# Kernel tuning notes

Measured on AMD Instinct MI355X. Metric: run time of the kernel, lower is better.

The kernel has to match this reference:

```python
import jax, jax.numpy as jnp
import numpy as np

# dims: N sentences, L tokens each, M=2 memory slots/sentence, D hidden, H heads
N, L, M, D, H, FF, V, P, LAYERS = 4, 256, 2, 768, 12, 3072, 32000, 1024, 4
DH = D // H


def setup_inputs() -> dict:
    key = jax.random.key(0)
    ks = jax.random.split(key, 20)
    s = 0.02
    inp = {
        'input_ids': jax.random.randint(ks[0], (N, L), 0, V),
        'memory': jax.random.normal(ks[1], (N, M, D), jnp.float32),
        'emb_table': jax.random.normal(ks[2], (V, D), jnp.float32) * s,
        'pos_table': jax.random.normal(ks[3], (P + 2, D), jnp.float32) * s,
        'Wq': jax.random.normal(ks[4], (LAYERS, D, D), jnp.float32) * s,
        'bq': jnp.zeros((LAYERS, D), jnp.float32),
        'Wk': jax.random.normal(ks[5], (LAYERS, D, D), jnp.float32) * s,
        'bk': jnp.zeros((LAYERS, D), jnp.float32),
        'Wv': jax.random.normal(ks[6], (LAYERS, D, D), jnp.float32) * s,
        'bv': jnp.zeros((LAYERS, D), jnp.float32),
        'W1': jax.random.normal(ks[7], (LAYERS, D, FF), jnp.float32) * s,
        'b1': jnp.zeros((LAYERS, FF), jnp.float32),
        'W2': jax.random.normal(ks[8], (LAYERS, FF, D), jnp.float32) * s,
        'b2': jnp.zeros((LAYERS, D), jnp.float32),
        'g1': jnp.ones((LAYERS, D), jnp.float32),
        'be1': jnp.zeros((LAYERS, D), jnp.float32),
        'g2': jnp.ones((LAYERS, D), jnp.float32),
        'be2': jnp.zeros((LAYERS, D), jnp.float32),
    }
    return inp


def _layer_norm(x, g, b):
    mu = jnp.mean(x, axis=-1, keepdims=True)
    var = jnp.mean((x - mu) ** 2, axis=-1, keepdims=True)
    return (x - mu) / jnp.sqrt(var + 1e-5) * g + b


def _encoder(input_ids, memory, emb_table, pos_table, Wq, bq, Wk, bk, Wv, bv,
             W1, b1, W2, b2, g1, be1, g2, be2):
    base = N * M            # token rows start here in the packed input
    T = base + N * L        # total rows (memory rows + token rows)
    Kk = M + L              # keys per query (own memory + own tokens)

    # position embeddings: memory rows get pos (p % M); tokens get id_pos + M
    mem_pos = jnp.tile(jnp.arange(M), N)                    # (N*M,)
    mem = memory.reshape(N * M, D) + pos_table[mem_pos]
    fwd_pos = jnp.tile(jnp.arange(L) + M, N)                # (N*L,)
    tok = emb_table[input_ids.reshape(-1)] + pos_table[fwd_pos]
    x = jnp.concatenate([mem, tok], axis=0)                 # (T, D)

    # per-sentence key set: its M memory rows then its L token rows
    key_pos = jnp.concatenate([
        jnp.arange(N)[:, None] * M + jnp.arange(M)[None, :],
        base + jnp.arange(N)[:, None] * L + jnp.arange(L)[None, :],
    ], axis=1)                                              # (N, Kk)
    sent = jnp.concatenate([jnp.repeat(jnp.arange(N), M),
                            jnp.repeat(jnp.arange(N), L)])  # (T,)
    gidx = key_pos[sent]                                    # (T, Kk)
    # equal-length sentences => the additive mask built by the torch code is
    # all zeros (key_len == max_key_len for every row), so it is omitted.

    scale = 1.0 / np.sqrt(DH)
    for i in range(LAYERS):
        # K/V are linear row-wise, so project once on all rows then gather
        # (identical math to projecting the gathered tgt, without T-fold GEMM)
        q = (x @ Wq[i] + bq[i]).reshape(T, H, DH)
        kf = (x @ Wk[i] + bk[i]).reshape(T, H, DH)
        vf = (x @ Wv[i] + bv[i]).reshape(T, H, DH)
        kg = kf[gidx]                                       # (T, Kk, H, DH)
        vg = vf[gidx]
        scores = jnp.einsum('thd,tkhd->thk', q, kg) * scale
        probs = jax.nn.softmax(scores, axis=-1)
        ctx = jnp.einsum('thk,tkhd->thd', probs, vg).reshape(T, D)
        x = _layer_norm(x + ctx, g1[i], be1[i])
        h = jax.nn.gelu(x @ W1[i] + b1[i], approximate=False)
        x = _layer_norm(x + h @ W2[i] + b2[i], g2[i], be2[i])

    ret = key_pos[:, M:]                                    # (N, L) token rows
    return x[ret]                                           # (N, L, D)


def reference(input_ids, memory, emb_table, pos_table, Wq, bq, Wk, bk, Wv, bv,
              W1, b1, W2, b2, g1, be1, g2, be2):
    return _encoder(input_ids, memory, emb_table, pos_table, Wq, bq, Wk, bk,
                    Wv, bv, W1, b1, W2, b2, g1, be1, g2, be2)
```

## Files before the change

### kernel.cpp

```cpp
#include <hip/hip_runtime.h>
#include <hip/hip_bf16.h>
#include <math.h>

#define N_      4
#define L_      256
#define M_      2
#define D_      768
#define H_      12
#define FF_     3072
#define DH_     64
#define LAYERS_ 4
#define BASE_   8
#define T_      1032
#define TP_     1088
#define KK_     258
#define QS_     2304
#define PS_     264

typedef __bf16 bf16x8 __attribute__((ext_vector_type(8)));
typedef float  f32x4  __attribute__((ext_vector_type(4)));

__device__ __forceinline__ void async_load16(const __hip_bfloat16* g, __hip_bfloat16* l) {
  __builtin_amdgcn_global_load_lds(
      (const __attribute__((address_space(1))) unsigned int*)g,
      (__attribute__((address_space(3))) unsigned int*)l, 16, 0, 0);
}

#define PP_QKV_END_ 6912
#define PP_W1_END_  16128
#define PP_W2_END_  25344
#define PP_B_END_   25380
#define PP_TOTAL_   26412

__global__ __launch_bounds__(256) void preprocess_kernel(
    const float* __restrict__ Wq, const float* __restrict__ Wk,
    const float* __restrict__ Wv, const float* __restrict__ W1,
    const float* __restrict__ W2,
    const float* __restrict__ bq, const float* __restrict__ bk,
    const float* __restrict__ bv,
    const int* __restrict__ ids, const float* __restrict__ memory,
    const float* __restrict__ emb, const float* __restrict__ pos,
    __hip_bfloat16* __restrict__ Wqkvt, __hip_bfloat16* __restrict__ W1t,
    __hip_bfloat16* __restrict__ W2t, float* __restrict__ bqkv,
    float* __restrict__ x, __hip_bfloat16* __restrict__ xb) {
  __shared__ float tile[32][33];
  const int bid = blockIdx.x;
  const int tid = threadIdx.x;

  const float* src;
  __hip_bfloat16* dst;
  int K, N, bx, by;

  if (bid < PP_QKV_END_) {
    int l = bid / 1728, r = bid - l * 1728;
    int which = r / 576; r -= which * 576;
    by = r / 24; bx = r - by * 24;
    src = (which == 0 ? Wq : which == 1 ? Wk : Wv) + (size_t)l * D_ * D_;
    dst = Wqkvt + (size_t)l * QS_ * D_ + (size_t)which * D_ * D_;
    K = D_; N = D_;
  } else if (bid < PP_W1_END_) {
    int r0 = bid - PP_QKV_END_;
    int l = r0 / 2304, r = r0 - l * 2304;
    by = r / 96; bx = r - by * 96;
    src = W1 + (size_t)l * D_ * FF_;
    dst = W1t + (size_t)l * FF_ * D_;
    K = D_; N = FF_;
  } else if (bid < PP_W2_END_) {
    int r0 = bid - PP_W1_END_;
    int l = r0 / 2304, r = r0 - l * 2304;
    by = r / 24; bx = r - by * 24;
    src = W2 + (size_t)l * FF_ * D_;
    dst = W2t + (size_t)l * D_ * FF_;
    K = FF_; N = D_;
  } else if (bid < PP_B_END_) {
    int i = (bid - PP_W2_END_) * 256 + tid;
    int l = i / QS_, j = i - l * QS_;
    float v;
    if (j < D_)            v = bq[l * D_ + j];
    else if (j < 2 * D_)   v = bk[l * D_ + (j - D_)];
    else                   v = bv[l * D_ + (j - 2 * D_)];
    bqkv[i] = v;
    return;
  } else {
    int row = bid - PP_B_END_;
    const float *s2, *p;
    if (row < BASE_) {
      s2 = memory + (long long)row * D_;
      p  = pos + (row & 1) * D_;
    } else {
      int i = row - BASE_;
      int tok = ids[i];
      s2 = emb + (long long)tok * D_;
      p  = pos + (M_ + (i & (L_ - 1))) * D_;
    }
    for (int d = tid; d < D_; d += 256) {
      float v = s2[d] + p[d];
      x[(long long)row * D_ + d]  = v;
      xb[(long long)row * D_ + d] = __float2bfloat16(v);
    }
    return;
  }

  const int k0 = by * 32, n0 = bx * 32;
  const int r = tid >> 5, c = tid & 31;
  #pragma unroll
  for (int i = 0; i < 4; ++i)
    tile[r + i * 8][c] = src[(size_t)(k0 + r + i * 8) * N + n0 + c];
  __syncthreads();
  #pragma unroll
  for (int i = 0; i < 4; ++i)
    dst[(size_t)(n0 + r + i * 8) * K + k0 + c] = __float2bfloat16(tile[c][r + i * 8]);
}

template <int ACT, int WF32, int WBF16, int WVT>
__global__ __launch_bounds__(256) void gemm_mfma(
    const __hip_bfloat16* __restrict__ A,
    const __hip_bfloat16* __restrict__ Bt,
    const float* __restrict__ bias,
    float* __restrict__ C,
    __hip_bfloat16* __restrict__ Cb,
    __hip_bfloat16* __restrict__ vt,
    int N, int K) {
  __shared__ __align__(16) __hip_bfloat16 As[4][64][32];
  __shared__ __align__(16) __hip_bfloat16 Bs[4][64][32];
  const int tid  = threadIdx.x;
  const int lane = tid & 63, wid = tid >> 6;
  const int ln   = lane & 15, qd = lane >> 4;
  const int wm   = wid >> 1, wn = wid & 1;

  const size_t arow = (size_t)(blockIdx.y * 64 + wid * 16 + (lane >> 2)) * K + (lane & 3) * 8;
  const size_t brow = (size_t)(blockIdx.x * 64 + wid * 16 + (lane >> 2)) * K + (lane & 3) * 8;

  f32x4 acc[2][2] = {};
  for (int k0 = 0; k0 < K; k0 += 128) {
    #pragma unroll
    for (int s = 0; s < 4; ++s) {
      async_load16(A  + arow + k0 + s * 32, &As[s][wid * 16][0]);
      async_load16(Bt + brow + k0 + s * 32, &Bs[s][wid * 16][0]);
    }
    __syncthreads();
    #pragma unroll
    for (int s = 0; s < 4; ++s) {
      bf16x8 a0 = *(const bf16x8*)&As[s][wm * 32 + ln][qd * 8];
      bf16x8 a1 = *(const bf16x8*)&As[s][wm * 32 + 16 + ln][qd * 8];
      bf16x8 b0 = *(const bf16x8*)&Bs[s][wn * 32 + ln][qd * 8];
      bf16x8 b1 = *(const bf16x8*)&Bs[s][wn * 32 + 16 + ln][qd * 8];
      acc[0][0] = __builtin_amdgcn_mfma_f32_16x16x32_bf16(a0, b0, acc[0][0], 0, 0, 0);
      acc[0][1] = __builtin_amdgcn_mfma_f32_16x16x32_bf16(a0, b1, acc[0][1], 0, 0, 0);
      acc[1][0] = __builtin_amdgcn_mfma_f32_16x16x32_bf16(a1, b0, acc[1][0], 0, 0, 0);
      acc[1][1] = __builtin_amdgcn_mfma_f32_16x16x32_bf16(a1, b1, acc[1][1], 0, 0, 0);
    }
    __syncthreads();
  }
  #pragma unroll
  for (int mt = 0; mt < 2; ++mt) {
    #pragma unroll
    for (int nt = 0; nt < 2; ++nt) {
      const int col = blockIdx.x * 64 + wn * 32 + nt * 16 + ln;
      const float bv = bias[col];
      #pragma unroll
      for (int i = 0; i < 4; ++i) {
        const int row = blockIdx.y * 64 + wm * 32 + mt * 16 + qd * 4 + i;
        float v = acc[mt][nt][i] + bv;
        if (ACT) v = 0.5f * v * (1.f + erff(v * 0.70710678118654752f));
        if (WF32)  C[(size_t)row * N + col]  = v;
        if (WVT) {
          if (col < 2 * D_) Cb[(size_t)row * N + col] = __float2bfloat16(v);
          else              vt[(size_t)(col - 2 * D_) * TP_ + row] = __float2bfloat16(v);
        } else if (WBF16) {
          Cb[(size_t)row * N + col] = __float2bfloat16(v);
        }
      }
    }
  }
}

__global__ __launch_bounds__(256) void attn_mfma(
    const __hip_bfloat16* __restrict__ qkv,
    const __hip_bfloat16* __restrict__ vtb,
    float* __restrict__ ctx) {
  __shared__ __align__(16) __hip_bfloat16 Ps[64][PS_];
  const int qt = blockIdx.x, h = blockIdx.y, b = blockIdx.z;
  const int tid = threadIdx.x;
  const int w = tid >> 6, lane = tid & 63, ln = lane & 15, qd = lane >> 4;

  bf16x8 aq0, aq1;
  {
    int j = qt * 64 + w * 16 + ln;
    int tok = (j < 256) ? (BASE_ + b * L_ + j)
            : ((j < KK_) ? (b * M_ + (j - 256)) : (b * M_));
    const __hip_bfloat16* qp = qkv + (size_t)tok * QS_ + h * DH_ + qd * 8;
    aq0 = *(const bf16x8*)qp;
    aq1 = *(const bf16x8*)(qp + 32);
  }

  f32x4 sa[17];
  #pragma unroll
  for (int nt = 0; nt < 17; ++nt) sa[nt] = (f32x4){0.f, 0.f, 0.f, 0.f};
  #pragma unroll
  for (int nt = 0; nt < 17; ++nt) {
    int key = nt * 16 + ln;
    int ktok = (key < 256) ? (BASE_ + b * L_ + key)
             : ((key < KK_) ? (b * M_ + (key - 256)) : (b * M_));
    const __hip_bfloat16* kp = qkv + (size_t)ktok * QS_ + D_ + h * DH_ + qd * 8;
    bf16x8 b0 = *(const bf16x8*)kp;
    bf16x8 b1 = *(const bf16x8*)(kp + 32);
    sa[nt] = __builtin_amdgcn_mfma_f32_16x16x32_bf16(aq0, b0, sa[nt], 0, 0, 0);
    sa[nt] = __builtin_amdgcn_mfma_f32_16x16x32_bf16(aq1, b1, sa[nt], 0, 0, 0);
  }

  #pragma unroll
  for (int i = 0; i < 4; ++i) {
    float v[17];
    #pragma unroll
    for (int nt = 0; nt < 17; ++nt) v[nt] = sa[nt][i] * 0.125f;
    float mx = -1e30f;
    #pragma unroll
    for (int nt = 0; nt < 16; ++nt) mx = fmaxf(mx, v[nt]);
    if (ln < 2) mx = fmaxf(mx, v[16]);
    #pragma unroll
    for (int m = 1; m < 16; m <<= 1) mx = fmaxf(mx, __shfl_xor(mx, m));
    float sum = 0.f;
    #pragma unroll
    for (int nt = 0; nt < 17; ++nt) {
      float e = (nt == 16 && ln >= 2) ? 0.f : __expf(v[nt] - mx);
      v[nt] = e;
      sum += e;
    }
    #pragma unroll
    for (int m = 1; m < 16; m <<= 1) sum += __shfl_xor(sum, m);
    float is = 1.f / sum;
    const int row = w * 16 + qd * 4 + i;
    #pragma unroll
    for (int nt = 0; nt < 17; ++nt)
      if (nt < 16 || ln < 2)
        Ps[row][nt * 16 + ln] = __float2bfloat16(v[nt] * is);
  }

  f32x4 oa[4] = {};
  #pragma unroll
  for (int k0 = 0; k0 < 8; ++k0) {
    bf16x8 ap = *(const bf16x8*)&Ps[w * 16 + ln][k0 * 32 + qd * 8];
    #pragma unroll
    for (int nt = 0; nt < 4; ++nt) {
      const __hip_bfloat16* vp = vtb + (size_t)(h * DH_ + nt * 16 + ln) * TP_
                               + BASE_ + b * L_ + k0 * 32 + qd * 8;
      bf16x8 bv = *(const bf16x8*)vp;
      oa[nt] = __builtin_amdgcn_mfma_f32_16x16x32_bf16(ap, bv, oa[nt], 0, 0, 0);
    }
  }
  {
    float p0[4], p1[4];
    #pragma unroll
    for (int i = 0; i < 4; ++i) {
      p0[i] = __bfloat162float(Ps[w * 16 + qd * 4 + i][256]);
      p1[i] = __bfloat162float(Ps[w * 16 + qd * 4 + i][257]);
    }
    #pragma unroll
    for (int nt = 0; nt < 4; ++nt) {
      const __hip_bfloat16* vp = vtb + (size_t)(h * DH_ + nt * 16 + ln) * TP_ + b * M_;
      float v0 = __bfloat162float(vp[0]);
      float v1 = __bfloat162float(vp[1]);
      #pragma unroll
      for (int i = 0; i < 4; ++i) oa[nt][i] += p0[i] * v0 + p1[i] * v1;
    }
  }

  #pragma unroll
  for (int i = 0; i < 4; ++i) {
    int j = qt * 64 + w * 16 + qd * 4 + i;
    if (j < KK_) {
      int tok = (j < 256) ? (BASE_ + b * L_ + j) : (b * M_ + (j - 256));
      #pragma unroll
      for (int nt = 0; nt < 4; ++nt)
        ctx[(size_t)tok * D_ + h * DH_ + nt * 16 + ln] = oa[nt][i];
    }
  }
}

__global__ __launch_bounds__(256) void add_ln_kernel(
    float* __restrict__ x, const float* __restrict__ delta,
    const float* __restrict__ g, const float* __restrict__ b,
    __hip_bfloat16* __restrict__ xb, float* __restrict__ out) {
  __shared__ float sred[4];
  __shared__ float sbc;
  const int t = blockIdx.x, tid = threadIdx.x;
  float y[3];
  float s = 0.f;
  #pragma unroll
  for (int i = 0; i < 3; ++i) {
    int d = tid + i * 256;
    y[i] = x[(long long)t * D_ + d] + delta[(long long)t * D_ + d];
    s += y[i];
  }
  #pragma unroll
  for (int o = 32; o > 0; o >>= 1) s += __shfl_down(s, o);
  if ((tid & 63) == 0) sred[tid >> 6] = s;
  __syncthreads();
  if (tid == 0) sbc = (sred[0] + sred[1] + sred[2] + sred[3]) * (1.f / D_);
  __syncthreads();
  const float mu = sbc;
  __syncthreads();
  float vs = 0.f;
  #pragma unroll
  for (int i = 0; i < 3; ++i) { float d = y[i] - mu; vs += d * d; }
  #pragma unroll
  for (int o = 32; o > 0; o >>= 1) vs += __shfl_down(vs, o);
  if ((tid & 63) == 0) sred[tid >> 6] = vs;
  __syncthreads();
  if (tid == 0) sbc = (sred[0] + sred[1] + sred[2] + sred[3]) * (1.f / D_);
  __syncthreads();
  const float inv = rsqrtf(sbc + 1e-5f);
  #pragma unroll
  for (int i = 0; i < 3; ++i) {
    int d = tid + i * 256;
    float v = (y[i] - mu) * inv * g[d] + b[d];
    x[(long long)t * D_ + d]  = v;
    xb[(long long)t * D_ + d] = __float2bfloat16(v);
    if (out != nullptr && t >= BASE_)
      out[(size_t)(t - BASE_) * D_ + d] = v;
  }
}

extern "C" void kernel_launch(void* const* d_in, const int* in_sizes, int n_in,
                              void* d_out, int out_size, void* d_ws, size_t ws_size,
                              hipStream_t stream) {
  const int*   ids    = (const int*)  d_in[0];
  const float* memory = (const float*)d_in[1];
  const float* emb    = (const float*)d_in[2];
  const float* pos    = (const float*)d_in[3];
  const float* Wq     = (const float*)d_in[4];
  const float* bq     = (const float*)d_in[5];
  const float* Wk     = (const float*)d_in[6];
  const float* bk     = (const float*)d_in[7];
  const float* Wv     = (const float*)d_in[8];
  const float* bv     = (const float*)d_in[9];
  const float* W1     = (const float*)d_in[10];
  const float* b1     = (const float*)d_in[11];
  const float* W2     = (const float*)d_in[12];
  const float* b2     = (const float*)d_in[13];
  const float* g1     = (const float*)d_in[14];
  const float* be1    = (const float*)d_in[15];
  const float* g2     = (const float*)d_in[16];
  const float* be2    = (const float*)d_in[17];

  char* w = (char*)d_ws;
  float* x    = (float*)w;                      w += (size_t)TP_ * D_ * 4;
  float* cb   = (float*)w;                      w += (size_t)TP_ * D_ * 4;
  float* bqkv = (float*)w;                      w += (size_t)LAYERS_ * QS_ * 4;
  __hip_bfloat16* xb    = (__hip_bfloat16*)w;   w += (size_t)TP_ * D_ * 2;
  __hip_bfloat16* qkvb  = (__hip_bfloat16*)w;   w += (size_t)TP_ * QS_ * 2;
  __hip_bfloat16* vtb   = (__hip_bfloat16*)w;   w += (size_t)D_ * TP_ * 2;
  __hip_bfloat16* hbb   = (__hip_bfloat16*)w;   w += (size_t)TP_ * FF_ * 2;
  __hip_bfloat16* Wqkvt = (__hip_bfloat16*)w;   w += (size_t)LAYERS_ * QS_ * D_ * 2;
  __hip_bfloat16* W1t   = (__hip_bfloat16*)w;   w += (size_t)LAYERS_ * FF_ * D_ * 2;
  __hip_bfloat16* W2t   = (__hip_bfloat16*)w;   w += (size_t)LAYERS_ * D_ * FF_ * 2;

  preprocess_kernel<<<PP_TOTAL_, 256, 0, stream>>>(
      Wq, Wk, Wv, W1, W2, bq, bk, bv, ids, memory, emb, pos,
      Wqkvt, W1t, W2t, bqkv, x, xb);

  for (int i = 0; i < LAYERS_; ++i) {
    gemm_mfma<0, 0, 1, 1><<<dim3(QS_ / 64, TP_ / 64), 256, 0, stream>>>(
        xb, Wqkvt + (size_t)i * QS_ * D_, bqkv + i * QS_, nullptr, qkvb, vtb, QS_, D_);
    attn_mfma<<<dim3(5, H_, N_), 256, 0, stream>>>(qkvb, vtb, cb);
    add_ln_kernel<<<T_, 256, 0, stream>>>(x, cb, g1 + i * D_, be1 + i * D_, xb, nullptr);
    gemm_mfma<1, 0, 1, 0><<<dim3(FF_ / 64, TP_ / 64), 256, 0, stream>>>(
        xb, W1t + (size_t)i * FF_ * D_, b1 + i * FF_, nullptr, hbb, nullptr, FF_, D_);
    gemm_mfma<0, 1, 0, 0><<<dim3(D_ / 64, TP_ / 64), 256, 0, stream>>>(
        hbb, W2t + (size_t)i * D_ * FF_, b2 + i * D_, cb, nullptr, nullptr, D_, FF_);
    add_ln_kernel<<<T_, 256, 0, stream>>>(
        x, cb, g2 + i * D_, be2 + i * D_, xb,
        (i == LAYERS_ - 1) ? (float*)d_out : nullptr);
  }
}
```

Measured before the change: 562.5 us.

## Double-buffer GEMM LDS staging and split-K the W2 projection

Adds a second LDS buffer so the next 128-wide K tile is loaded asynchronously while MFMAs consume the current one. The W2 GEMM is additionally split into two K halves across blockIdx.z, writing separate fp32 partials. The following add+layernorm kernel sums them, which raises block count for the small-N GEMM. This costs doubled LDS per block, an extra partial buffer, and extra memory traffic in the layernorm.

```diff
diff --git a/kernel.cpp b/kernel.cpp
--- a/kernel.cpp
+++ b/kernel.cpp
@@ -112,7 +112,7 @@
     dst[(size_t)(n0 + r + i * 8) * K + k0 + c] = __float2bfloat16(tile[c][r + i * 8]);
 }
 
-template <int ACT, int WF32, int WBF16, int WVT>
+template <int ACT, int WF32, int WBF16, int WVT, int NSPLIT>
 __global__ __launch_bounds__(256) void gemm_mfma(
     const __hip_bfloat16* __restrict__ A,
     const __hip_bfloat16* __restrict__ Bt,
@@ -120,50 +120,64 @@
     float* __restrict__ C,
     __hip_bfloat16* __restrict__ Cb,
     __hip_bfloat16* __restrict__ vt,
-    int N, int K) {
-  __shared__ __align__(16) __hip_bfloat16 As[4][64][32];
-  __shared__ __align__(16) __hip_bfloat16 Bs[4][64][32];
+    int N, int Ktot) {
+  __shared__ __align__(16) __hip_bfloat16 As[2][4][64][32];
+  __shared__ __align__(16) __hip_bfloat16 Bs[2][4][64][32];
   const int tid  = threadIdx.x;
   const int lane = tid & 63, wid = tid >> 6;
   const int ln   = lane & 15, qd = lane >> 4;
   const int wm   = wid >> 1, wn = wid & 1;
 
-  const size_t arow = (size_t)(blockIdx.y * 64 + wid * 16 + (lane >> 2)) * K + (lane & 3) * 8;
-  const size_t brow = (size_t)(blockIdx.x * 64 + wid * 16 + (lane >> 2)) * K + (lane & 3) * 8;
+  const int K = Ktot / NSPLIT;
+  const size_t koff = (size_t)blockIdx.z * K;
+
+  const size_t arow = (size_t)(blockIdx.y * 64 + wid * 16 + (lane >> 2)) * Ktot + koff + (lane & 3) * 8;
+  const size_t brow = (size_t)(blockIdx.x * 64 + wid * 16 + (lane >> 2)) * Ktot + koff + (lane & 3) * 8;
 
   f32x4 acc[2][2] = {};
+
+#define STAGE(b, k0) do {                                                     \
+    _Pragma("unroll")                                                         \
+    for (int s_ = 0; s_ < 4; ++s_) {                                          \
+      async_load16(A  + arow + (k0) + s_ * 32, &As[b][s_][wid * 16][0]);      \
+      async_load16(Bt + brow + (k0) + s_ * 32, &Bs[b][s_][wid * 16][0]);      \
+    }                                                                         \
+  } while (0)
+
+  STAGE(0, 0);
+  __syncthreads();
+  int buf = 0;
   for (int k0 = 0; k0 < K; k0 += 128) {
+    if (k0 + 128 < K) STAGE(buf ^ 1, k0 + 128);
     #pragma unroll
     for (int s = 0; s < 4; ++s) {
-      async_load16(A  + arow + k0 + s * 32, &As[s][wid * 16][0]);
-      async_load16(Bt + brow + k0 + s * 32, &Bs[s][wid * 16][0]);
-    }
-    __syncthreads();
-    #pragma unroll
-    for (int s = 0; s < 4; ++s) {
-      bf16x8 a0 = *(const bf16x8*)&As[s][wm * 32 + ln][qd * 8];
-      bf16x8 a1 = *(const bf16x8*)&As[s][wm * 32 + 16 + ln][qd * 8];
-      bf16x8 b0 = *(const bf16x8*)&Bs[s][wn * 32 + ln][qd * 8];
-      bf16x8 b1 = *(const bf16x8*)&Bs[s][wn * 32 + 16 + ln][qd * 8];
+      bf16x8 a0 = *(const bf16x8*)&As[buf][s][wm * 32 + ln][qd * 8];
+      bf16x8 a1 = *(const bf16x8*)&As[buf][s][wm * 32 + 16 + ln][qd * 8];
+      bf16x8 b0 = *(const bf16x8*)&Bs[buf][s][wn * 32 + ln][qd * 8];
+      bf16x8 b1 = *(const bf16x8*)&Bs[buf][s][wn * 32 + 16 + ln][qd * 8];
       acc[0][0] = __builtin_amdgcn_mfma_f32_16x16x32_bf16(a0, b0, acc[0][0], 0, 0, 0);
       acc[0][1] = __builtin_amdgcn_mfma_f32_16x16x32_bf16(a0, b1, acc[0][1], 0, 0, 0);
       acc[1][0] = __builtin_amdgcn_mfma_f32_16x16x32_bf16(a1, b0, acc[1][0], 0, 0, 0);
       acc[1][1] = __builtin_amdgcn_mfma_f32_16x16x32_bf16(a1, b1, acc[1][1], 0, 0, 0);
     }
     __syncthreads();
-  }
+    buf ^= 1;
+  }
+#undef STAGE
+
   #pragma unroll
   for (int mt = 0; mt < 2; ++mt) {
     #pragma unroll
     for (int nt = 0; nt < 2; ++nt) {
       const int col = blockIdx.x * 64 + wn * 32 + nt * 16 + ln;
-      const float bv = bias[col];
+      const float bv = (NSPLIT == 1 || blockIdx.z == 0) ? bias[col] : 0.f;
       #pragma unroll
       for (int i = 0; i < 4; ++i) {
         const int row = blockIdx.y * 64 + wm * 32 + mt * 16 + qd * 4 + i;
         float v = acc[mt][nt][i] + bv;
         if (ACT) v = 0.5f * v * (1.f + erff(v * 0.70710678118654752f));
-        if (WF32)  C[(size_t)row * N + col]  = v;
+        if (WF32)
+          C[(size_t)blockIdx.z * TP_ * N + (size_t)row * N + col] = v;
         if (WVT) {
           if (col < 2 * D_) Cb[(size_t)row * N + col] = __float2bfloat16(v);
           else              vt[(size_t)(col - 2 * D_) * TP_ + row] = __float2bfloat16(v);
@@ -278,6 +292,7 @@
   }
 }
 
+template <int NS>
 __global__ __launch_bounds__(256) void add_ln_kernel(
     float* __restrict__ x, const float* __restrict__ delta,
     const float* __restrict__ g, const float* __restrict__ b,
@@ -290,8 +305,12 @@
   #pragma unroll
   for (int i = 0; i < 3; ++i) {
     int d = tid + i * 256;
-    y[i] = x[(long long)t * D_ + d] + delta[(long long)t * D_ + d];
-    s += y[i];
+    float v = x[(long long)t * D_ + d];
+    #pragma unroll
+    for (int s2 = 0; s2 < NS; ++s2)
+      v += delta[(size_t)s2 * TP_ * D_ + (long long)t * D_ + d];
+    y[i] = v;
+    s += v;
   }
   #pragma unroll
   for (int o = 32; o > 0; o >>= 1) s += __shfl_down(s, o);
@@ -346,7 +365,7 @@
 
   char* w = (char*)d_ws;
   float* x    = (float*)w;                      w += (size_t)TP_ * D_ * 4;
-  float* cb   = (float*)w;                      w += (size_t)TP_ * D_ * 4;
+  float* cb   = (float*)w;                      w += (size_t)2 * TP_ * D_ * 4;
   float* bqkv = (float*)w;                      w += (size_t)LAYERS_ * QS_ * 4;
   __hip_bfloat16* xb    = (__hip_bfloat16*)w;   w += (size_t)TP_ * D_ * 2;
   __hip_bfloat16* qkvb  = (__hip_bfloat16*)w;   w += (size_t)TP_ * QS_ * 2;
@@ -361,15 +380,15 @@
       Wqkvt, W1t, W2t, bqkv, x, xb);
 
   for (int i = 0; i < LAYERS_; ++i) {
-    gemm_mfma<0, 0, 1, 1><<<dim3(QS_ / 64, TP_ / 64), 256, 0, stream>>>(
+    gemm_mfma<0, 0, 1, 1, 1><<<dim3(QS_ / 64, TP_ / 64), 256, 0, stream>>>(
         xb, Wqkvt + (size_t)i * QS_ * D_, bqkv + i * QS_, nullptr, qkvb, vtb, QS_, D_);
     attn_mfma<<<dim3(5, H_, N_), 256, 0, stream>>>(qkvb, vtb, cb);
-    add_ln_kernel<<<T_, 256, 0, stream>>>(x, cb, g1 + i * D_, be1 + i * D_, xb, nullptr);
-    gemm_mfma<1, 0, 1, 0><<<dim3(FF_ / 64, TP_ / 64), 256, 0, stream>>>(
+    add_ln_kernel<1><<<T_, 256, 0, stream>>>(x, cb, g1 + i * D_, be1 + i * D_, xb, nullptr);
+    gemm_mfma<1, 0, 1, 0, 1><<<dim3(FF_ / 64, TP_ / 64), 256, 0, stream>>>(
         xb, W1t + (size_t)i * FF_ * D_, b1 + i * FF_, nullptr, hbb, nullptr, FF_, D_);
-    gemm_mfma<0, 1, 0, 0><<<dim3(D_ / 64, TP_ / 64), 256, 0, stream>>>(
+    gemm_mfma<0, 1, 0, 0, 2><<<dim3(D_ / 64, TP_ / 64, 2), 256, 0, stream>>>(
         hbb, W2t + (size_t)i * D_ * FF_, b2 + i * D_, cb, nullptr, nullptr, D_, FF_);
-    add_ln_kernel<<<T_, 256, 0, stream>>>(
+    add_ln_kernel<2><<<T_, 256, 0, stream>>>(
         x, cb, g2 + i * D_, be2 + i * D_, xb,
         (i == LAYERS_ - 1) ? (float*)d_out : nullptr);
   }
```

Result: faster. 544.5 us (-3.2%).
